# Optimization experiments

Measured on AMD Instinct MI355X. Metric: run time of the kernel, lower is better.

## Reference

```python
import jax, jax.numpy as jnp
import numpy as np

D = 1024
H = 16
DH = D // H  # 64
B, S = 4, 1024


def setup_inputs() -> dict:
    key = jax.random.key(0)
    ks = jax.random.split(key, 7)
    sequences = jax.random.normal(ks[0], (B, S, D), dtype=jnp.float32)
    scale = 1.0 / np.sqrt(DH)
    Wq = jax.random.normal(ks[1], (H, DH, DH), dtype=jnp.float32) * scale
    Wk = jax.random.normal(ks[2], (H, DH, DH), dtype=jnp.float32) * scale
    Wv = jax.random.normal(ks[3], (H, DH, DH), dtype=jnp.float32) * scale
    bq = jax.random.normal(ks[4], (H, DH), dtype=jnp.float32) * 0.01
    bk = jax.random.normal(ks[5], (H, DH), dtype=jnp.float32) * 0.01
    bv = jax.random.normal(ks[6], (H, DH), dtype=jnp.float32) * 0.01
    return {"sequences": sequences, "Wq": Wq, "Wk": Wk, "Wv": Wv,
            "bq": bq, "bk": bk, "bv": bv}


def reference(sequences, Wq, Wk, Wv, bq, bk, bv):
    b, s, d = sequences.shape
    x = sequences.reshape(b, s, H, DH)  # split channels into heads
    # per-head Linear: y = x @ W.T + b (torch convention)
    q = jnp.einsum('bshd,hed->bshe', x, Wq) + bq
    k = jnp.einsum('bshd,hed->bshe', x, Wk) + bk
    v = jnp.einsum('bshd,hed->bshe', x, Wv) + bv
    inv_sqrt_dh = jnp.asarray(1.0 / np.sqrt(DH), dtype=sequences.dtype)
    scores = jnp.einsum('bshe,bthe->bhst', q, k) * inv_sqrt_dh  # [B,H,S,S]
    attn = jax.nn.softmax(scores, axis=-1)
    out = jnp.einsum('bhst,bthe->bshe', attn, v)  # [B,S,H,DH]
    return out.reshape(b, s, d)  # hstack of heads == reshape here
```

## Files before the change

kernel.cpp:

```cpp
#include <hip/hip_runtime.h>

#define H 16
#define DH 64
#define BB 4
#define SS 1024
#define DD 1024

typedef __attribute__((ext_vector_type(8))) short bf16x8;
typedef __attribute__((ext_vector_type(4))) float f32x4;
typedef __attribute__((ext_vector_type(4))) unsigned int u32x4;
typedef _Float16 f16x4 __attribute__((ext_vector_type(4)));
typedef _Float16 f16x8 __attribute__((ext_vector_type(8)));
typedef __fp16 hf16x2 __attribute__((ext_vector_type(2)));

#define QSCALE 0.18033688011112042f

__device__ __forceinline__ unsigned short f2bf(float f) {
    union { float f; unsigned u; } v; v.f = f;
    unsigned u = v.u;
    return (unsigned short)((u + 0x7FFFu + ((u >> 16) & 1u)) >> 16);
}

__device__ __forceinline__ unsigned short f2h(float f) {
    union { _Float16 h; unsigned short u; } v;
    v.h = (_Float16)f;
    return v.u;
}

__device__ __forceinline__ void pack8(unsigned short* dst, f32x4 a, f32x4 b) {
    unsigned u0 = (unsigned)f2bf(a[0]) | ((unsigned)f2bf(a[1]) << 16);
    unsigned u1 = (unsigned)f2bf(a[2]) | ((unsigned)f2bf(a[3]) << 16);
    unsigned u2 = (unsigned)f2bf(b[0]) | ((unsigned)f2bf(b[1]) << 16);
    unsigned u3 = (unsigned)f2bf(b[2]) | ((unsigned)f2bf(b[3]) << 16);
    u32x4 v = {u0, u1, u2, u3};
    *(u32x4*)dst = v;
}

__device__ __forceinline__ void async_cp1k(const unsigned short* g,
                                           unsigned short* l, int lane) {
    __builtin_amdgcn_global_load_lds(
        (const __attribute__((address_space(1))) unsigned int*)(g + lane * 8),
        (__attribute__((address_space(3))) unsigned int*)l, 16, 0, 0);
}

__global__ __launch_bounds__(256) void wprep_kernel(
    const float* __restrict__ Wq, const float* __restrict__ Wk,
    const float* __restrict__ Wv, unsigned short* __restrict__ Wp)
{
    const int tg = blockIdx.x * 256 + threadIdx.x;
    const int r = tg >> 2, part = tg & 3;
    const int e = r & 63, hm = r >> 6;
    const int m = hm % 3, h = hm / 3;
    const float* src = (m == 0 ? Wq : (m == 1 ? Wk : Wv)) +
                       (size_t)(h * 64 + e) * 64 + part * 16;
    const float scale = (m == 0) ? QSCALE : 1.0f;
    f32x4 f0 = ((const f32x4*)src)[0];
    f32x4 f1 = ((const f32x4*)src)[1];
    f32x4 f2 = ((const f32x4*)src)[2];
    f32x4 f3 = ((const f32x4*)src)[3];
    f0 *= scale; f1 *= scale; f2 *= scale; f3 *= scale;
    unsigned short tmp[16];
    pack8(tmp, f0, f1);
    pack8(tmp + 8, f2, f3);
    unsigned short* dst = Wp + (size_t)(hm * 64 + e) * 64;
    const int c0 = part * 2, sw = e & 7;
    *(u32x4*)(dst + (c0 ^ sw) * 8)       = *(const u32x4*)tmp;
    *(u32x4*)(dst + ((c0 + 1) ^ sw) * 8) = *(const u32x4*)(tmp + 8);
}

__global__ __launch_bounds__(256) void qkv_kernel(
    const float* __restrict__ x, const unsigned short* __restrict__ Wp,
    const float* __restrict__ bq, const float* __restrict__ bk,
    const float* __restrict__ bv,
    unsigned short* __restrict__ Qg, unsigned short* __restrict__ Kg,
    unsigned short* __restrict__ VTg)
{
    __shared__ __align__(16) unsigned short Xl[4096];
    __shared__ __align__(16) unsigned short Wl[12288];

    const int bid = blockIdx.x;
    const int sc = bid & 15, h = (bid >> 4) & 15, b = bid >> 8;
    const int s0 = sc * 64;
    const int tid = threadIdx.x;
    const int lane = tid & 63, w = tid >> 6;

    {
        const unsigned short* wbase = Wp + (size_t)h * 12288;
#pragma unroll
        for (int sub = 0; sub < 6; sub++) {
            const int off = w * 3072 + sub * 512;
            async_cp1k(wbase + off, &Wl[off], lane);
        }
    }
    {
        const int s = tid >> 2, part = tid & 3;
        const float* src = x + ((size_t)(b * SS + s0 + s)) * DD + h * DH + part * 16;
        f32x4 f0 = ((const f32x4*)src)[0];
        f32x4 f1 = ((const f32x4*)src)[1];
        f32x4 f2 = ((const f32x4*)src)[2];
        f32x4 f3 = ((const f32x4*)src)[3];
        unsigned short tmp[16];
        pack8(tmp, f0, f1);
        pack8(tmp + 8, f2, f3);
        const int c0 = part * 2, sws = s & 7;
        *(u32x4*)&Xl[s * 64 + (c0 ^ sws) * 8]       = *(const u32x4*)tmp;
        *(u32x4*)&Xl[s * 64 + ((c0 + 1) ^ sws) * 8] = *(const u32x4*)(tmp + 8);
    }
    __syncthreads();

    const int l15 = lane & 15, quad = lane >> 4, sw = l15 & 7;

    f32x4 acc[3][4];
#pragma unroll
    for (int m = 0; m < 3; m++)
#pragma unroll
        for (int nt = 0; nt < 4; nt++) acc[m][nt] = (f32x4){0.f, 0.f, 0.f, 0.f};

#pragma unroll
    for (int k2 = 0; k2 < 2; k2++) {
        const int csw = (((k2 << 2) | quad) ^ sw) * 8;
        bf16x8 a = *(const bf16x8*)&Xl[(w * 16 + l15) * 64 + csw];
#pragma unroll
        for (int nt = 0; nt < 4; nt++) {
            const int boff = (nt * 16 + l15) * 64 + csw;
            bf16x8 b0 = *(const bf16x8*)&Wl[boff];
            acc[0][nt] = __builtin_amdgcn_mfma_f32_16x16x32_bf16(a, b0, acc[0][nt], 0, 0, 0);
            bf16x8 b1 = *(const bf16x8*)&Wl[4096 + boff];
            acc[1][nt] = __builtin_amdgcn_mfma_f32_16x16x32_bf16(a, b1, acc[1][nt], 0, 0, 0);
            bf16x8 b2 = *(const bf16x8*)&Wl[8192 + boff];
            acc[2][nt] = __builtin_amdgcn_mfma_f32_16x16x32_bf16(a, b2, acc[2][nt], 0, 0, 0);
        }
    }
    __syncthreads();

#pragma unroll
    for (int nt = 0; nt < 4; nt++) {
        const int e = nt * 16 + l15;
        const float bqs = bq[h * DH + e] * QSCALE;
        const float bks = bk[h * DH + e];
        const float bvs = bv[h * DH + e];
#pragma unroll
        for (int r = 0; r < 4; r++) {
            const int srow = w * 16 + quad * 4 + r;
            Xl[srow * 64 + e] = f2bf(acc[0][nt][r] + bqs);
            Wl[srow * 64 + e] = f2bf(acc[1][nt][r] + bks);
            Wl[4096 + e * 64 + quad * 16 + w * 4 + r] = f2h(acc[2][nt][r] + bvs);
        }
    }
    __syncthreads();
    {
        const size_t bh = (size_t)(b * H + h);
        const int row = tid >> 2, part = tid & 3;
        const int cg = part * 16, c0 = part * 2, swr = row & 7;
        unsigned short* qdst = Qg + (bh * SS + s0 + row) * DH + cg;
        *(u32x4*)qdst       = *(const u32x4*)&Xl[row * 64 + cg];
        *(u32x4*)(qdst + 8) = *(const u32x4*)&Xl[row * 64 + cg + 8];
        unsigned short* kbase = Kg + (bh * 16 + sc) * 4096 + row * 64;
        *(u32x4*)(kbase + (c0 ^ swr) * 8)       = *(const u32x4*)&Wl[row * 64 + c0 * 8];
        *(u32x4*)(kbase + ((c0 + 1) ^ swr) * 8) = *(const u32x4*)&Wl[row * 64 + c0 * 8 + 8];
        unsigned short* vbase = VTg + (bh * 16 + sc) * 4096 + row * 64;
        *(u32x4*)(vbase + (c0 ^ swr) * 8)       = *(const u32x4*)&Wl[4096 + row * 64 + c0 * 8];
        *(u32x4*)(vbase + ((c0 + 1) ^ swr) * 8) = *(const u32x4*)&Wl[4096 + row * 64 + c0 * 8 + 8];
    }
}

__global__ __launch_bounds__(256) void attn_kernel(
    const unsigned short* __restrict__ Qg, const unsigned short* __restrict__ Kg,
    const unsigned short* __restrict__ VTg, float* __restrict__ out)
{
    __shared__ __align__(16) unsigned short Kl0[4096], Kl1[4096];
    __shared__ __align__(16) unsigned short Vl0[4096], Vl1[4096];

    const int bid = blockIdx.x;
    const int bh = bid & 63, qg = bid >> 6;
    const int h = bh & 15, b = bh >> 4;
    const int tid = threadIdx.x;
    const int lane = tid & 63, w = tid >> 6;
    const int l15 = lane & 15, quad = lane >> 4, sw = l15 & 7;

    const unsigned short* Kt = Kg + (size_t)bh * 16 * 4096;
    const unsigned short* Vt = VTg + (size_t)bh * 16 * 4096;

    const int kb0 = l15 * 64 + ((quad)     ^ sw) * 8;
    const int kb1 = l15 * 64 + ((4 | quad) ^ sw) * 8;
    const int vb0 = l15 * 64 + (((quad << 1))     ^ sw) * 8;
    const int vb1 = l15 * 64 + (((quad << 1) | 1) ^ sw) * 8;

    bf16x8 aQ[2][2];
#pragma unroll
    for (int j = 0; j < 2; j++) {
        const int qrow = (qg * 2 + j) * 64 + w * 16 + l15;
        const unsigned short* qp = Qg + ((size_t)bh * SS + qrow) * DH + quad * 8;
        aQ[j][0] = *(const bf16x8*)(qp);
        aQ[j][1] = *(const bf16x8*)(qp + 32);
    }

    {
        const int off = w * 1024;
        async_cp1k(Kt + off,       Kl0 + off,       lane);
        async_cp1k(Kt + off + 512, Kl0 + off + 512, lane);
        async_cp1k(Vt + off,       Vl0 + off,       lane);
        async_cp1k(Vt + off + 512, Vl0 + off + 512, lane);
    }

    f32x4 accO[2][4];
#pragma unroll
    for (int j = 0; j < 2; j++)
#pragma unroll
        for (int et = 0; et < 4; et++) accO[j][et] = (f32x4){0.f, 0.f, 0.f, 0.f};
    float rs_acc[2] = {0.f, 0.f};

    auto step = [&](int kt, const unsigned short* Kc, const unsigned short* Vc,
                    unsigned short* Kn, unsigned short* Vn) {
        __syncthreads();
        if (kt < 15) {
            const unsigned short* kg = Kt + (kt + 1) * 4096;
            const unsigned short* vg = Vt + (kt + 1) * 4096;
            const int off = w * 1024;
            async_cp1k(kg + off,       Kn + off,       lane);
            async_cp1k(kg + off + 512, Kn + off + 512, lane);
            async_cp1k(vg + off,       Vn + off,       lane);
            async_cp1k(vg + off + 512, Vn + off + 512, lane);
        }

        bf16x8 aK[4][2];
#pragma unroll
        for (int nt = 0; nt < 4; nt++) {
            aK[nt][0] = *(const bf16x8*)(Kc + kb0 + nt * 1024);
            aK[nt][1] = *(const bf16x8*)(Kc + kb1 + nt * 1024);
        }
        f16x8 aV01[4], aV23[4];
#pragma unroll
        for (int et = 0; et < 4; et++) {
            aV01[et] = *(const f16x8*)(Vc + vb0 + et * 1024);
            aV23[et] = *(const f16x8*)(Vc + vb1 + et * 1024);
        }

        f32x4 sc[2][4];
#pragma unroll
        for (int j = 0; j < 2; j++)
#pragma unroll
            for (int nt = 0; nt < 4; nt++) {
                f32x4 z = {0.f, 0.f, 0.f, 0.f};
                z = __builtin_amdgcn_mfma_f32_16x16x32_bf16(aK[nt][0], aQ[j][0], z, 0, 0, 0);
                z = __builtin_amdgcn_mfma_f32_16x16x32_bf16(aK[nt][1], aQ[j][1], z, 0, 0, 0);
                sc[j][nt] = z;
            }

#pragma unroll
        for (int j = 0; j < 2; j++) {
            float rs = 0.f;
            f16x4 pf[4];
#pragma unroll
            for (int nt = 0; nt < 4; nt++) {
                float p0 = exp2f(sc[j][nt][0]);
                float p1 = exp2f(sc[j][nt][1]);
                float p2 = exp2f(sc[j][nt][2]);
                float p3 = exp2f(sc[j][nt][3]);
                rs += (p0 + p1) + (p2 + p3);
                union { hf16x2 h; unsigned u; } lo, hi;
                lo.h = __builtin_amdgcn_cvt_pkrtz(p0, p1);
                hi.h = __builtin_amdgcn_cvt_pkrtz(p2, p3);
                union { unsigned u[2]; f16x4 v; } pk;
                pk.u[0] = lo.u; pk.u[1] = hi.u;
                pf[nt] = pk.v;
            }
            rs_acc[j] += rs;

#pragma unroll
            for (int et = 0; et < 4; et++) {
                f16x4 v0 = __builtin_shufflevector(aV01[et], aV01[et], 0, 1, 2, 3);
                f16x4 v1 = __builtin_shufflevector(aV01[et], aV01[et], 4, 5, 6, 7);
                f16x4 v2 = __builtin_shufflevector(aV23[et], aV23[et], 0, 1, 2, 3);
                f16x4 v3 = __builtin_shufflevector(aV23[et], aV23[et], 4, 5, 6, 7);
                accO[j][et] = __builtin_amdgcn_mfma_f32_16x16x16f16(v0, pf[0], accO[j][et], 0, 0, 0);
                accO[j][et] = __builtin_amdgcn_mfma_f32_16x16x16f16(v1, pf[1], accO[j][et], 0, 0, 0);
                accO[j][et] = __builtin_amdgcn_mfma_f32_16x16x16f16(v2, pf[2], accO[j][et], 0, 0, 0);
                accO[j][et] = __builtin_amdgcn_mfma_f32_16x16x16f16(v3, pf[3], accO[j][et], 0, 0, 0);
            }
        }
    };

    for (int i = 0; i < 8; i++) {
        step(2 * i,     Kl0, Vl0, Kl1, Vl1);
        step(2 * i + 1, Kl1, Vl1, Kl0, Vl0);
    }

#pragma unroll
    for (int j = 0; j < 2; j++) {
        float rs = rs_acc[j];
        rs += __shfl_xor(rs, 16);
        rs += __shfl_xor(rs, 32);
        const float inv = 1.0f / rs;
        const int srow = (qg * 2 + j) * 64 + w * 16 + l15;
        float* op = out + ((size_t)b * SS + srow) * DD + h * DH;
#pragma unroll
        for (int et = 0; et < 4; et++) {
            f32x4 v = accO[j][et] * inv;
            *(f32x4*)(op + et * 16 + quad * 4) = v;
        }
    }
}

extern "C" void kernel_launch(void* const* d_in, const int* in_sizes, int n_in,
                              void* d_out, int out_size, void* d_ws, size_t ws_size,
                              hipStream_t stream) {
    const float* x  = (const float*)d_in[0];
    const float* Wq = (const float*)d_in[1];
    const float* Wk = (const float*)d_in[2];
    const float* Wv = (const float*)d_in[3];
    const float* bq = (const float*)d_in[4];
    const float* bk = (const float*)d_in[5];
    const float* bv = (const float*)d_in[6];

    const size_t NE = (size_t)BB * H * SS * DH;
    unsigned short* Qg  = (unsigned short*)d_ws;
    unsigned short* Kg  = Qg + NE;
    unsigned short* VTg = Kg + NE;
    unsigned short* Wp  = VTg + NE;

    wprep_kernel<<<48, 256, 0, stream>>>(Wq, Wk, Wv, Wp);
    qkv_kernel<<<BB * H * (SS / 64), 256, 0, stream>>>(x, Wp, bq, bk, bv,
                                                       Qg, Kg, VTg);
    attn_kernel<<<BB * H * 8, 256, 0, stream>>>(Qg, Kg, VTg, (float*)d_out);
}
```

Before: 120.6 us.

## Halve query rows per attention block, double grid, use native exp2

```diff
diff --git a/kernel.cpp b/kernel.cpp
--- a/kernel.cpp
+++ b/kernel.cpp
@@ -14,6 +14,18 @@
 typedef __fp16 hf16x2 __attribute__((ext_vector_type(2)));
 
 #define QSCALE 0.18033688011112042f
+
+#if __has_builtin(__builtin_amdgcn_exp2f)
+__device__ __forceinline__ float fast_exp2(float x) {
+    return __builtin_amdgcn_exp2f(x);
+}
+#else
+__device__ __forceinline__ float fast_exp2(float x) {
+    float r;
+    asm("v_exp_f32 %0, %1" : "=v"(r) : "v"(x));
+    return r;
+}
+#endif
 
 __device__ __forceinline__ unsigned short f2bf(float f) {
     union { float f; unsigned u; } v; v.f = f;
@@ -172,7 +184,7 @@
     __shared__ __align__(16) unsigned short Vl0[4096], Vl1[4096];
 
     const int bid = blockIdx.x;
-    const int bh = bid & 63, qg = bid >> 6;
+    const int bh = bid & 63, qt = bid >> 6;
     const int h = bh & 15, b = bh >> 4;
     const int tid = threadIdx.x;
     const int lane = tid & 63, w = tid >> 6;
@@ -186,13 +198,12 @@
     const int vb0 = l15 * 64 + (((quad << 1))     ^ sw) * 8;
     const int vb1 = l15 * 64 + (((quad << 1) | 1) ^ sw) * 8;
 
-    bf16x8 aQ[2][2];
-#pragma unroll
-    for (int j = 0; j < 2; j++) {
-        const int qrow = (qg * 2 + j) * 64 + w * 16 + l15;
+    bf16x8 aQ0, aQ1;
+    {
+        const int qrow = qt * 64 + w * 16 + l15;
         const unsigned short* qp = Qg + ((size_t)bh * SS + qrow) * DH + quad * 8;
-        aQ[j][0] = *(const bf16x8*)(qp);
-        aQ[j][1] = *(const bf16x8*)(qp + 32);
+        aQ0 = *(const bf16x8*)(qp);
+        aQ1 = *(const bf16x8*)(qp + 32);
     }
 
     {
@@ -203,12 +214,10 @@
         async_cp1k(Vt + off + 512, Vl0 + off + 512, lane);
     }
 
-    f32x4 accO[2][4];
-#pragma unroll
-    for (int j = 0; j < 2; j++)
-#pragma unroll
-        for (int et = 0; et < 4; et++) accO[j][et] = (f32x4){0.f, 0.f, 0.f, 0.f};
-    float rs_acc[2] = {0.f, 0.f};
+    f32x4 accO[4];
+#pragma unroll
+    for (int et = 0; et < 4; et++) accO[et] = (f32x4){0.f, 0.f, 0.f, 0.f};
+    float rs_acc = 0.f;
 
     auto step = [&](int kt, const unsigned short* Kc, const unsigned short* Vc,
                     unsigned short* Kn, unsigned short* Vn) {
@@ -236,48 +245,43 @@
             aV23[et] = *(const f16x8*)(Vc + vb1 + et * 1024);
         }
 
-        f32x4 sc[2][4];
-#pragma unroll
-        for (int j = 0; j < 2; j++)
-#pragma unroll
-            for (int nt = 0; nt < 4; nt++) {
-                f32x4 z = {0.f, 0.f, 0.f, 0.f};
-                z = __builtin_amdgcn_mfma_f32_16x16x32_bf16(aK[nt][0], aQ[j][0], z, 0, 0, 0);
-                z = __builtin_amdgcn_mfma_f32_16x16x32_bf16(aK[nt][1], aQ[j][1], z, 0, 0, 0);
-                sc[j][nt] = z;
-            }
-
-#pragma unroll
-        for (int j = 0; j < 2; j++) {
-            float rs = 0.f;
-            f16x4 pf[4];
-#pragma unroll
-            for (int nt = 0; nt < 4; nt++) {
-                float p0 = exp2f(sc[j][nt][0]);
-                float p1 = exp2f(sc[j][nt][1]);
-                float p2 = exp2f(sc[j][nt][2]);
-                float p3 = exp2f(sc[j][nt][3]);
-                rs += (p0 + p1) + (p2 + p3);
-                union { hf16x2 h; unsigned u; } lo, hi;
-                lo.h = __builtin_amdgcn_cvt_pkrtz(p0, p1);
-                hi.h = __builtin_amdgcn_cvt_pkrtz(p2, p3);
-                union { unsigned u[2]; f16x4 v; } pk;
-                pk.u[0] = lo.u; pk.u[1] = hi.u;
-                pf[nt] = pk.v;
-            }
-            rs_acc[j] += rs;
-
-#pragma unroll
-            for (int et = 0; et < 4; et++) {
-                f16x4 v0 = __builtin_shufflevector(aV01[et], aV01[et], 0, 1, 2, 3);
-                f16x4 v1 = __builtin_shufflevector(aV01[et], aV01[et], 4, 5, 6, 7);
-                f16x4 v2 = __builtin_shufflevector(aV23[et], aV23[et], 0, 1, 2, 3);
-                f16x4 v3 = __builtin_shufflevector(aV23[et], aV23[et], 4, 5, 6, 7);
-                accO[j][et] = __builtin_amdgcn_mfma_f32_16x16x16f16(v0, pf[0], accO[j][et], 0, 0, 0);
-                accO[j][et] = __builtin_amdgcn_mfma_f32_16x16x16f16(v1, pf[1], accO[j][et], 0, 0, 0);
-                accO[j][et] = __builtin_amdgcn_mfma_f32_16x16x16f16(v2, pf[2], accO[j][et], 0, 0, 0);
-                accO[j][et] = __builtin_amdgcn_mfma_f32_16x16x16f16(v3, pf[3], accO[j][et], 0, 0, 0);
-            }
+        f32x4 sc[4];
+#pragma unroll
+        for (int nt = 0; nt < 4; nt++) {
+            f32x4 z = {0.f, 0.f, 0.f, 0.f};
+            z = __builtin_amdgcn_mfma_f32_16x16x32_bf16(aK[nt][0], aQ0, z, 0, 0, 0);
+            z = __builtin_amdgcn_mfma_f32_16x16x32_bf16(aK[nt][1], aQ1, z, 0, 0, 0);
+            sc[nt] = z;
+        }
+
+        float rs = 0.f;
+        f16x4 pf[4];
+#pragma unroll
+        for (int nt = 0; nt < 4; nt++) {
+            float p0 = fast_exp2(sc[nt][0]);
+            float p1 = fast_exp2(sc[nt][1]);
+            float p2 = fast_exp2(sc[nt][2]);
+            float p3 = fast_exp2(sc[nt][3]);
+            rs += (p0 + p1) + (p2 + p3);
+            union { hf16x2 h; unsigned u; } lo, hi;
+            lo.h = __builtin_amdgcn_cvt_pkrtz(p0, p1);
+            hi.h = __builtin_amdgcn_cvt_pkrtz(p2, p3);
+            union { unsigned u[2]; f16x4 v; } pk;
+            pk.u[0] = lo.u; pk.u[1] = hi.u;
+            pf[nt] = pk.v;
+        }
+        rs_acc += rs;
+
+#pragma unroll
+        for (int et = 0; et < 4; et++) {
+            f16x4 v0 = __builtin_shufflevector(aV01[et], aV01[et], 0, 1, 2, 3);
+            f16x4 v1 = __builtin_shufflevector(aV01[et], aV01[et], 4, 5, 6, 7);
+            f16x4 v2 = __builtin_shufflevector(aV23[et], aV23[et], 0, 1, 2, 3);
+            f16x4 v3 = __builtin_shufflevector(aV23[et], aV23[et], 4, 5, 6, 7);
+            accO[et] = __builtin_amdgcn_mfma_f32_16x16x16f16(v0, pf[0], accO[et], 0, 0, 0);
+            accO[et] = __builtin_amdgcn_mfma_f32_16x16x16f16(v1, pf[1], accO[et], 0, 0, 0);
+            accO[et] = __builtin_amdgcn_mfma_f32_16x16x16f16(v2, pf[2], accO[et], 0, 0, 0);
+            accO[et] = __builtin_amdgcn_mfma_f32_16x16x16f16(v3, pf[3], accO[et], 0, 0, 0);
         }
     };
 
@@ -286,17 +290,16 @@
         step(2 * i + 1, Kl1, Vl1, Kl0, Vl0);
     }
 
-#pragma unroll
-    for (int j = 0; j < 2; j++) {
-        float rs = rs_acc[j];
+    {
+        float rs = rs_acc;
         rs += __shfl_xor(rs, 16);
         rs += __shfl_xor(rs, 32);
         const float inv = 1.0f / rs;
-        const int srow = (qg * 2 + j) * 64 + w * 16 + l15;
+        const int srow = qt * 64 + w * 16 + l15;
         float* op = out + ((size_t)b * SS + srow) * DD + h * DH;
 #pragma unroll
         for (int et = 0; et < 4; et++) {
-            f32x4 v = accO[j][et] * inv;
+            f32x4 v = accO[et] * inv;
             *(f32x4*)(op + et * 16 + quad * 4) = v;
         }
     }
@@ -322,5 +325,5 @@
     wprep_kernel<<<48, 256, 0, stream>>>(Wq, Wk, Wv, Wp);
     qkv_kernel<<<BB * H * (SS / 64), 256, 0, stream>>>(x, Wp, bq, bk, bv,
                                                        Qg, Kg, VTg);
-    attn_kernel<<<BB * H * 8, 256, 0, stream>>>(Qg, Kg, VTg, (float*)d_out);
-}
+    attn_kernel<<<BB * H * 16, 256, 0, stream>>>(Qg, Kg, VTg, (float*)d_out);
+}
```

Measured after the change: 117.4 us. 2.6% less time.
